# Kernel tuning notes

Hardware: AMD Instinct MI355X
Metric: run time of the kernel (lower is better)

## Reference

```python
import jax, jax.numpy as jnp
import numpy as np

N_ITEMS = 1_000_000
N_FACTORS = 64

def setup_inputs() -> dict:
    key = jax.random.key(0)
    emb_weight = jax.random.normal(key, (N_ITEMS, N_FACTORS), dtype=jnp.float32)
    return {"emb_weight": emb_weight, "item_idx": 12345, "size": 50}

def reference(emb_weight, item_idx, size):
    # gather query row: u = emb(ind)  -> [d]
    u = emb_weight[item_idx]
    # scores = u @ emb.T  -> [n_items] (GEMV against full table)
    scores = emb_weight @ u
    # top-k retrieval (size <= n_items, clamp as in original)
    k = min(size, scores.shape[0])
    s, i = jax.lax.top_k(scores, k)
    return s, i
```

## Files before the change

kernel.cpp:

```cpp
#include <hip/hip_runtime.h>

#define NEG_INF (-1.0e30f)
#define CAP 4096
#define NBKT 4096

__device__ __forceinline__ unsigned flip(float f) {
    unsigned u = __float_as_uint(f);
    return (u & 0x80000000u) ? ~u : (u | 0x80000000u);
}

__device__ __forceinline__ bool pair_gt(float sa, int ia, float sb, int ib) {
    return (sa > sb) || (sa == sb && ia < ib);
}

__global__ __launch_bounds__(256) void k_gemv_hist(const float* __restrict__ emb,
                                                   const int* __restrict__ p_idx,
                                                   int n_items,
                                                   float* __restrict__ scores,
                                                   unsigned* __restrict__ hist) {
    __shared__ unsigned h[NBKT];
    const int tid = threadIdx.x;
    for (int i = tid; i < NBKT; i += 256) h[i] = 0;

    const float4* uq = (const float4*)(emb + (size_t)(*p_idx) * 64);
    float4 u[16];
#pragma unroll
    for (int c = 0; c < 16; ++c) u[c] = uq[c];
    __syncthreads();

    const int stride = gridDim.x * 256;
    for (int row = blockIdx.x * 256 + tid; row < n_items; row += stride) {
        const float4* rp = (const float4*)(emb + (size_t)row * 64);
        float acc = 0.0f;
#pragma unroll
        for (int c = 0; c < 16; ++c) {
            const float4 r = rp[c];
            acc += r.x * u[c].x + r.y * u[c].y + r.z * u[c].z + r.w * u[c].w;
        }
        scores[row] = acc;
        atomicAdd(&h[flip(acc) >> 20], 1u);
    }

    __syncthreads();
    for (int i = tid; i < NBKT; i += 256) {
        const unsigned c = h[i];
        if (c) atomicAdd(&hist[i], c);
    }
}

__global__ __launch_bounds__(256) void k_compact(const float* __restrict__ scores,
                                                 int n4,
                                                 const unsigned* __restrict__ hist,
                                                 int k,
                                                 unsigned* __restrict__ cnt,
                                                 float* __restrict__ cand_s,
                                                 int* __restrict__ cand_i) {
    __shared__ unsigned h[NBKT];
    __shared__ unsigned psum[256];
    __shared__ unsigned sB;
    const int tid = threadIdx.x;
    for (int i = tid; i < NBKT; i += 256) h[i] = hist[i];
    __syncthreads();
    const int base = tid * 16;
    unsigned local = 0;
#pragma unroll
    for (int j = 0; j < 16; ++j) local += h[base + j];
    psum[tid] = local;
    __syncthreads();
    for (int stride = 1; stride < 256; stride <<= 1) {
        unsigned add = (tid + stride < 256) ? psum[tid + stride] : 0u;
        __syncthreads();
        psum[tid] += add;
        __syncthreads();
    }
    unsigned c = (tid + 1 < 256) ? psum[tid + 1] : 0u;
    for (int j = 15; j >= 0; --j) {
        unsigned hb = h[base + j];
        if (c < (unsigned)k && c + hb >= (unsigned)k) sB = (unsigned)(base + j);
        c += hb;
    }
    __syncthreads();
    const unsigned B = sB;

    const float4* s4 = (const float4*)scores;
    for (int i = blockIdx.x * 256 + tid; i < n4; i += gridDim.x * 256) {
        float4 v = s4[i];
        const float vv[4] = {v.x, v.y, v.z, v.w};
#pragma unroll
        for (int j = 0; j < 4; ++j) {
            if ((flip(vv[j]) >> 20) >= B) {
                unsigned pos = atomicAdd(cnt, 1u);
                if (pos < CAP) { cand_s[pos] = vv[j]; cand_i[pos] = i * 4 + j; }
            }
        }
    }
}

__global__ __launch_bounds__(256) void k_final(const float* __restrict__ cand_s,
                                               const int* __restrict__ cand_i,
                                               const unsigned* __restrict__ cnt,
                                               int k, float* __restrict__ out) {
    __shared__ float ss[CAP];
    __shared__ int   si[CAP];
    const int tid = threadIdx.x;
    unsigned c = *cnt;
    const int n = (c > CAP) ? CAP : (int)c;
    int N = 64; while (N < n) N <<= 1;
    for (int i = tid; i < N; i += 256) {
        const bool v = i < n;
        ss[i] = v ? cand_s[i] : NEG_INF;
        si[i] = v ? cand_i[i] : 0x7fffffff;
    }
    __syncthreads();
    for (int kk = 2; kk <= N; kk <<= 1) {
        for (int j = kk >> 1; j > 0; j >>= 1) {
            for (int i = tid; i < N; i += 256) {
                int l = i ^ j;
                if (l > i) {
                    float s_i = ss[i], s_l = ss[l];
                    int   d_i = si[i], d_l = si[l];
                    bool sw = ((i & kk) == 0) ? pair_gt(s_l, d_l, s_i, d_i)
                                              : pair_gt(s_i, d_i, s_l, d_l);
                    if (sw) { ss[i] = s_l; si[i] = d_l; ss[l] = s_i; si[l] = d_i; }
                }
            }
            __syncthreads();
        }
    }
    if (tid < k) {
        out[tid]     = ss[tid];
        out[k + tid] = (float)si[tid];
    }
}

extern "C" void kernel_launch(void* const* d_in, const int* in_sizes, int n_in,
                              void* d_out, int out_size, void* d_ws, size_t ws_size,
                              hipStream_t stream) {
    const float* emb   = (const float*)d_in[0];
    const int*   p_idx = (const int*)d_in[1];
    const int n_items  = in_sizes[0] / 64;
    const int k        = out_size / 2;

    float*    scores = (float*)d_ws;
    unsigned* hist   = (unsigned*)(scores + n_items);
    unsigned* cnt    = hist + NBKT;
    float*    cand_s = (float*)(cnt + 1);
    int*      cand_i = (int*)(cand_s + CAP);

    hipMemsetAsync(hist, 0, (NBKT + 1) * sizeof(unsigned), stream);

    const int n4 = n_items / 4;
    k_gemv_hist<<<1024, 256, 0, stream>>>(emb, p_idx, n_items, scores, hist);
    k_compact  <<<256,  256, 0, stream>>>(scores, n4, hist, k, cnt, cand_s, cand_i);
    k_final    <<<1,    256, 0, stream>>>(cand_s, cand_i, cnt, k, (float*)d_out);
}
```

Measured before the change: 370.5 us.

## Fuse compaction and final sort via last-block pattern; enlarge GEMV grid

Merges the candidate compaction and the final bitonic sort into one kernel, where the last block to finish (tracked by an atomic done counter) performs the sort. This removes one kernel launch and its gap. It also raises the GEMV grid from 1024 to 2560 blocks, so each thread handles fewer rows and more loads are in flight, and lowers the compaction grid to 128 blocks. In exchange, every compaction block now reserves about 48KB of shared memory for the sort buffers, which may reduce occupancy, and correctness relies on the fences around the done counter.

```diff
diff --git a/kernel.cpp b/kernel.cpp
--- a/kernel.cpp
+++ b/kernel.cpp
@@ -3,6 +3,7 @@
 #define NEG_INF (-1.0e30f)
 #define CAP 4096
 #define NBKT 4096
+#define GEMV_GRID 2560
 
 __device__ __forceinline__ unsigned flip(float f) {
     unsigned u = __float_as_uint(f);
@@ -28,7 +29,7 @@
     for (int c = 0; c < 16; ++c) u[c] = uq[c];
     __syncthreads();
 
-    const int stride = gridDim.x * 256;
+    const int stride = GEMV_GRID * 256;
     for (int row = blockIdx.x * 256 + tid; row < n_items; row += stride) {
         const float4* rp = (const float4*)(emb + (size_t)row * 64);
         float acc = 0.0f;
@@ -48,17 +49,23 @@
     }
 }
 
-__global__ __launch_bounds__(256) void k_compact(const float* __restrict__ scores,
-                                                 int n4,
-                                                 const unsigned* __restrict__ hist,
-                                                 int k,
-                                                 unsigned* __restrict__ cnt,
-                                                 float* __restrict__ cand_s,
-                                                 int* __restrict__ cand_i) {
+__global__ __launch_bounds__(256) void k_compact_final(const float* __restrict__ scores,
+                                                       int n4,
+                                                       const unsigned* __restrict__ hist,
+                                                       int k,
+                                                       unsigned* __restrict__ cnt,
+                                                       unsigned* __restrict__ done,
+                                                       float* __restrict__ cand_s,
+                                                       int* __restrict__ cand_i,
+                                                       float* __restrict__ out) {
     __shared__ unsigned h[NBKT];
     __shared__ unsigned psum[256];
     __shared__ unsigned sB;
+    __shared__ int      s_last;
+    __shared__ float    ss[CAP];
+    __shared__ int      si[CAP];
     const int tid = threadIdx.x;
+
     for (int i = tid; i < NBKT; i += 256) h[i] = hist[i];
     __syncthreads();
     const int base = tid * 16;
@@ -94,17 +101,15 @@
             }
         }
     }
-}
 
-__global__ __launch_bounds__(256) void k_final(const float* __restrict__ cand_s,
-                                               const int* __restrict__ cand_i,
-                                               const unsigned* __restrict__ cnt,
-                                               int k, float* __restrict__ out) {
-    __shared__ float ss[CAP];
-    __shared__ int   si[CAP];
-    const int tid = threadIdx.x;
-    unsigned c = *cnt;
-    const int n = (c > CAP) ? CAP : (int)c;
+    __threadfence();
+    if (tid == 0) s_last = (atomicAdd(done, 1u) == gridDim.x - 1u);
+    __syncthreads();
+    if (!s_last) return;
+    __threadfence();
+
+    const unsigned cc = atomicAdd(cnt, 0u);
+    const int n = (cc > CAP) ? CAP : (int)cc;
     int N = 64; while (N < n) N <<= 1;
     for (int i = tid; i < N; i += 256) {
         const bool v = i < n;
@@ -144,13 +149,14 @@
     float*    scores = (float*)d_ws;
     unsigned* hist   = (unsigned*)(scores + n_items);
     unsigned* cnt    = hist + NBKT;
-    float*    cand_s = (float*)(cnt + 1);
+    unsigned* done   = cnt + 1;
+    float*    cand_s = (float*)(done + 1);
     int*      cand_i = (int*)(cand_s + CAP);
 
-    hipMemsetAsync(hist, 0, (NBKT + 1) * sizeof(unsigned), stream);
+    hipMemsetAsync(hist, 0, (NBKT + 2) * sizeof(unsigned), stream);
 
     const int n4 = n_items / 4;
-    k_gemv_hist<<<1024, 256, 0, stream>>>(emb, p_idx, n_items, scores, hist);
-    k_compact  <<<256,  256, 0, stream>>>(scores, n4, hist, k, cnt, cand_s, cand_i);
-    k_final    <<<1,    256, 0, stream>>>(cand_s, cand_i, cnt, k, (float*)d_out);
+    k_gemv_hist    <<<GEMV_GRID, 256, 0, stream>>>(emb, p_idx, n_items, scores, hist);
+    k_compact_final<<<128,       256, 0, stream>>>(scores, n4, hist, k, cnt, done,
+                                                   cand_s, cand_i, (float*)d_out);
 }
```

Result: slower. 382.1 us (+3.1%).
